# Performance work log

Measured on AMD Instinct MI355X. Metric: run time of the kernel, lower is better.

## Reference

```python
import jax, jax.numpy as jnp
import numpy as np

NUM_HEADS = 16

def _split_heads(x, H):
    B, S, D = x.shape
    return x.reshape(B, S, H, D // H).transpose(0, 2, 1, 3)  # [B,H,S,hd]

def _merge_heads(x):
    B, H, S, hd = x.shape
    return x.transpose(0, 2, 1, 3).reshape(B, S, H * hd)

def setup_inputs() -> dict:
    key = jax.random.key(0)
    k1, k2, k3, k4 = jax.random.split(key, 4)
    B, S, D = 2, 2048, 1024
    return {
        "visual_features": jax.random.normal(k1, (B, S, D), dtype=jnp.float32),
        "transaction_features": jax.random.normal(k2, (B, S, D), dtype=jnp.float32),
        "W_qkv": jax.random.normal(k3, (D, 3 * D), dtype=jnp.float32) * (1.0 / np.sqrt(D)),
        "W_out": jax.random.normal(k4, (D, D), dtype=jnp.float32) * (1.0 / np.sqrt(D)),
    }

def reference(visual_features, transaction_features, W_qkv, W_out):
    H = NUM_HEADS
    D = visual_features.shape[-1]
    scale = (D // H) ** -0.5

    v_q, v_k, v_v = [_split_heads(t, H) for t in jnp.split(visual_features @ W_qkv, 3, axis=-1)]
    t_q, t_k, t_v = [_split_heads(t, H) for t in jnp.split(transaction_features @ W_qkv, 3, axis=-1)]

    # visual queries attend to transaction keys/values (dropout = identity at eval)
    v2t = jax.nn.softmax(jnp.einsum('bhqd,bhkd->bhqk', v_q, t_k) * scale, axis=-1)
    t2v = jax.nn.softmax(jnp.einsum('bhqd,bhkd->bhqk', t_q, v_k) * scale, axis=-1)

    v2t_out = _merge_heads(jnp.einsum('bhqk,bhkd->bhqd', v2t, t_v))
    t2v_out = _merge_heads(jnp.einsum('bhqk,bhkd->bhqd', t2v, v_v))

    return (v2t_out + t2v_out) @ W_out
```

## Files before the change

### kernel.cpp

```cpp
#include <hip/hip_runtime.h>


typedef short  frag8 __attribute__((ext_vector_type(8)));
typedef float  f32x4 __attribute__((ext_vector_type(4)));

union F8 { frag8 f; uint2 u2[2]; unsigned u[4]; };

#define MFMA16(a,b,c) __builtin_amdgcn_mfma_f32_16x16x32_bf16((a),(b),(c),0,0,0)

__device__ __forceinline__ unsigned short f2bf(float f) {
  unsigned u = __builtin_bit_cast(unsigned, f);
  return (unsigned short)((u + 0x7fffu + ((u >> 16) & 1u)) >> 16);
}
__device__ __forceinline__ float bf2f(unsigned short s) {
  unsigned u = ((unsigned)s) << 16;
  return __builtin_bit_cast(float, u);
}
__device__ __forceinline__ unsigned pkbf(float lo, float hi) {
  unsigned r;
  asm("v_cvt_pk_bf16_f32 %0, %1, %2" : "=v"(r) : "v"(lo), "v"(hi));
  return r;
}
__device__ __forceinline__ float fexp2(float x) {
  float r;
  asm("v_exp_f32 %0, %1" : "=v"(r) : "v"(x));
  return r;
}

__global__ __launch_bounds__(256) void k_prep(
    const float* __restrict__ vis, const float* __restrict__ trn,
    unsigned short* __restrict__ Abf)
{
  size_t i8 = ((size_t)blockIdx.x * 256 + threadIdx.x) * 8;
  const float* src = (i8 < 4194304) ? vis + i8 : trn + (i8 - 4194304);
  float4 u = *(const float4*)src;
  float4 v = *(const float4*)(src + 4);
  uint4 w;
  w.x = pkbf(u.x, u.y); w.y = pkbf(u.z, u.w);
  w.z = pkbf(v.x, v.y); w.w = pkbf(v.z, v.w);
  *(uint4*)(Abf + i8) = w;
}

__global__ __launch_bounds__(256) void k_wt(
    const float* __restrict__ W, unsigned short* __restrict__ Wt, int N)
{
  __shared__ unsigned short L[64 * 72];
  const int tid = threadIdx.x;
  const int n0 = blockIdx.x * 64, k0 = blockIdx.y * 64;
  {
    int kr = tid >> 2, c4 = (tid & 3) * 16;
    const float* gp = W + (size_t)(k0 + kr) * N + n0 + c4;
    float4 u0 = *(const float4*)gp,       u1 = *(const float4*)(gp + 4);
    float4 u2 = *(const float4*)(gp + 8), u3 = *(const float4*)(gp + 12);
    unsigned* lw = (unsigned*)&L[kr * 72 + c4];
    lw[0] = pkbf(u0.x, u0.y); lw[1] = pkbf(u0.z, u0.w);
    lw[2] = pkbf(u1.x, u1.y); lw[3] = pkbf(u1.z, u1.w);
    lw[4] = pkbf(u2.x, u2.y); lw[5] = pkbf(u2.z, u2.w);
    lw[6] = pkbf(u3.x, u3.y); lw[7] = pkbf(u3.z, u3.w);
  }
  __syncthreads();
  int nr = tid >> 2, kc = (tid & 3) * 16;
  unsigned wb[8];
#pragma unroll
  for (int j = 0; j < 8; ++j) {
    unsigned lo = L[(kc + 2 * j)     * 72 + nr];
    unsigned hi = L[(kc + 2 * j + 1) * 72 + nr];
    wb[j] = lo | (hi << 16);
  }
  unsigned short* op = Wt + (size_t)(n0 + nr) * 1024 + k0 + kc;
  *(uint4*)op       = *(uint4*)&wb[0];
  *(uint4*)(op + 8) = *(uint4*)&wb[4];
}

__global__ __launch_bounds__(256) void k_gemm_qkv_b(
    const unsigned short* __restrict__ Abf, const unsigned short* __restrict__ WqbT,
    unsigned short* __restrict__ qkv)
{
  __shared__ unsigned short As_[128 * 32];
  __shared__ unsigned short Bs_[128 * 32];
  const int tid  = threadIdx.x;
  const int lane = tid & 63, wv = tid >> 6;
  const int lm = lane & 15, lg = lane >> 4;
  const int wg = (blockIdx.x & 7) * 192 + (blockIdx.x >> 3);
  const int nt = wg % 24, mt = wg / 24;
  const int wr = (wv >> 1) * 64, wc = (wv & 1) * 64;

  f32x4 acc[4][4] = {};

  const unsigned short* agp =
      Abf + (size_t)(mt * 128 + wv * 32 + (lane >> 2)) * 1024 + (lane & 3) * 8;
  const unsigned short* bgp =
      WqbT + (size_t)(nt * 128 + wv * 32 + (lane >> 2)) * 1024 + (lane & 3) * 8;

  for (int kt = 0; kt < 32; ++kt) {
    __syncthreads();
    __builtin_amdgcn_global_load_lds(
        (const __attribute__((address_space(1))) void*)(agp + kt * 32),
        (__attribute__((address_space(3))) void*)&As_[wv * 1024], 16, 0, 0);
    __builtin_amdgcn_global_load_lds(
        (const __attribute__((address_space(1))) void*)(agp + 16 * 1024 + kt * 32),
        (__attribute__((address_space(3))) void*)&As_[wv * 1024 + 512], 16, 0, 0);
    __builtin_amdgcn_global_load_lds(
        (const __attribute__((address_space(1))) void*)(bgp + kt * 32),
        (__attribute__((address_space(3))) void*)&Bs_[wv * 1024], 16, 0, 0);
    __builtin_amdgcn_global_load_lds(
        (const __attribute__((address_space(1))) void*)(bgp + 16 * 1024 + kt * 32),
        (__attribute__((address_space(3))) void*)&Bs_[wv * 1024 + 512], 16, 0, 0);
    __syncthreads();
    frag8 af[4], bfr[4];
#pragma unroll
    for (int mi = 0; mi < 4; ++mi)
      af[mi] = *(const frag8*)&As_[(wr + mi * 16 + lm) * 32 + lg * 8];
#pragma unroll
    for (int ni = 0; ni < 4; ++ni)
      bfr[ni] = *(const frag8*)&Bs_[(wc + ni * 16 + lm) * 32 + lg * 8];
#pragma unroll
    for (int mi = 0; mi < 4; ++mi)
#pragma unroll
      for (int ni = 0; ni < 4; ++ni)
        acc[mi][ni] = MFMA16(af[mi], bfr[ni], acc[mi][ni]);
  }

#pragma unroll
  for (int mi = 0; mi < 4; ++mi)
#pragma unroll
    for (int ni = 0; ni < 4; ++ni)
#pragma unroll
      for (int r = 0; r < 4; ++r) {
        int row = mt * 128 + wr + mi * 16 + lg * 4 + r;
        int col = nt * 128 + wc + ni * 16 + lm;
        qkv[(size_t)row * 3072 + col] = f2bf(acc[mi][ni][r]);
      }
}

__global__ __launch_bounds__(256) void k_vt(
    const unsigned short* __restrict__ qkv, unsigned short* __restrict__ Vt)
{
  __shared__ unsigned short L[64 * 72];
  const int tid = threadIdx.x;
  const int sblk = blockIdx.x;
  const int by = blockIdx.y;
  const int src = by >> 4, h = by & 15;
  {
    int sl = tid >> 2, dc = tid & 3;
    const unsigned short* gp =
        qkv + (size_t)(src * 2048 + sblk * 64 + sl) * 3072 + 2048 + h * 64 + dc * 16;
    *(frag8*)&L[sl * 72 + dc * 16]     = *(const frag8*)gp;
    *(frag8*)&L[sl * 72 + dc * 16 + 8] = *(const frag8*)(gp + 8);
  }
  __syncthreads();
  int d = tid >> 2, sc = tid & 3;
  unsigned wbuf[8];
#pragma unroll
  for (int j = 0; j < 8; ++j) {
    unsigned lo = L[(sc * 16 + 2 * j)     * 72 + d];
    unsigned hi = L[(sc * 16 + 2 * j + 1) * 72 + d];
    wbuf[j] = lo | (hi << 16);
  }
  unsigned short* op =
      Vt + ((size_t)(src * 16 + h) * 64 + d) * 2048 + sblk * 64 + sc * 16;
  *(uint4*)op       = *(uint4*)&wbuf[0];
  *(uint4*)(op + 8) = *(uint4*)&wbuf[4];
}

__global__ __launch_bounds__(256) void k_attn(
    const unsigned short* __restrict__ qkv, const unsigned short* __restrict__ Vt,
    unsigned short* __restrict__ Opart, float* __restrict__ lpart)
{
  __shared__ unsigned short Ks[2][32 * 72];
  __shared__ unsigned short Vs[2][8 * 272];
  const int tid  = threadIdx.x;
  const int lane = tid & 63, wv = tid >> 6;
  const int lm = lane & 15, lg = lane >> 4;
  const int qt = blockIdx.x, comb = blockIdx.y;
  const int dir = comb >> 5, bb = (comb >> 4) & 1, h = comb & 15;
  const int half = blockIdx.z;
  const int NT = 32, kt0 = half * 32;
  const int qbase  = (dir ? 4096 : 0) + bb * 2048;
  const int kvbase = (dir ? 0 : 4096) + bb * 2048;
  const int qcol = h * 64, kcol = 1024 + h * 64;

  const float QS = 0.125f * 1.44269504f;
  frag8 qf[2][2];
#pragma unroll
  for (int mi = 0; mi < 2; ++mi)
#pragma unroll
    for (int kb = 0; kb < 2; ++kb) {
      frag8 t = *(const frag8*)&qkv[
          (size_t)(qbase + qt * 128 + wv * 32 + mi * 16 + lm) * 3072 +
          qcol + kb * 32 + lg * 8];
#pragma unroll
      for (int j = 0; j < 8; ++j)
        t[j] = (short)f2bf(bf2f((unsigned short)t[j]) * QS);
      qf[mi][kb] = t;
    }

  f32x4 acc[2][4] = {};
  float lr[2] = {0.0f, 0.0f};

  const int skv = tid >> 3, sd = (tid & 7) * 8;
  const int vd = tid >> 2, vc = tid & 3;
  const unsigned short* __restrict__ kp =
      qkv + (size_t)(kvbase + skv) * 3072 + kcol + sd;
  const unsigned short* __restrict__ vtp =
      Vt + ((size_t)((kvbase >> 11) * 16 + h) * 64 + vd) * 2048 + vc * 8;

  frag8 Rk, Rv;

#define LOAD_R(kt_) do {                                                   \
    Rk = *(const frag8*)(kp + (size_t)(kt_) * (32 * 3072));                \
    Rv = *(const frag8*)(vtp + (size_t)(kt_) * 32);                        \
  } while (0)

#define WRITE_R(s_) do {                                                   \
    *(frag8*)&Ks[s_][skv * 72 + sd] = Rk;                                  \
    F8 tv_; tv_.f = Rv;                                                    \
    *(uint2*)&Vs[s_][(2 * vc) * 272 + vd * 4]     = tv_.u2[0];             \
    *(uint2*)&Vs[s_][(2 * vc + 1) * 272 + vd * 4] = tv_.u2[1];             \
  } while (0)

  LOAD_R(kt0);
  WRITE_R(0);
  LOAD_R(kt0 + 1);

  for (int i = 0; i < NT; ++i) {
    __syncthreads();
    if (i < NT - 1) WRITE_R((i + 1) & 1);
    if (i < NT - 2) LOAD_R(kt0 + i + 2);
    const int s = i & 1;

    frag8 kf[2][2];
#pragma unroll
    for (int t = 0; t < 2; ++t)
#pragma unroll
      for (int kb = 0; kb < 2; ++kb)
        kf[t][kb] = *(const frag8*)&Ks[s][(t * 16 + lm) * 72 + kb * 32 + lg * 8];
    f32x4 st[2][2] = {};
    __builtin_amdgcn_s_setprio(1);
#pragma unroll
    for (int mi = 0; mi < 2; ++mi)
#pragma unroll
      for (int t = 0; t < 2; ++t)
#pragma unroll
        for (int kb = 0; kb < 2; ++kb)
          st[mi][t] = MFMA16(kf[t][kb], qf[mi][kb], st[mi][t]);
    __builtin_amdgcn_s_setprio(0);

    frag8 pa[2];
#pragma unroll
    for (int mi = 0; mi < 2; ++mi) {
      f32x4 a = st[mi][0], b = st[mi][1];
      float p[8];
#pragma unroll
      for (int r = 0; r < 4; ++r) p[r]     = fexp2(a[r]);
#pragma unroll
      for (int r = 0; r < 4; ++r) p[4 + r] = fexp2(b[r]);
      lr[mi] += ((p[0] + p[1]) + (p[2] + p[3])) +
                ((p[4] + p[5]) + (p[6] + p[7]));
      F8 pk_;
      pk_.u[0] = pkbf(p[0], p[1]); pk_.u[1] = pkbf(p[2], p[3]);
      pk_.u[2] = pkbf(p[4], p[5]); pk_.u[3] = pkbf(p[6], p[7]);
      pa[mi] = pk_.f;
    }

    frag8 vb[4];
#pragma unroll
    for (int di = 0; di < 4; ++di) {
      F8 t;
      t.u2[0] = *(const uint2*)&Vs[s][lg * 272 + (di * 16 + lm) * 4];
      t.u2[1] = *(const uint2*)&Vs[s][(4 + lg) * 272 + (di * 16 + lm) * 4];
      vb[di] = t.f;
    }
    __builtin_amdgcn_s_setprio(1);
#pragma unroll
    for (int mi = 0; mi < 2; ++mi)
#pragma unroll
      for (int di = 0; di < 4; ++di)
        acc[mi][di] = MFMA16(pa[mi], vb[di], acc[mi][di]);
    __builtin_amdgcn_s_setprio(0);
  }

#undef LOAD_R
#undef WRITE_R

#pragma unroll
  for (int mi = 0; mi < 2; ++mi) {
    float l = lr[mi];
    l += __shfl_xor(l, 16);
    l += __shfl_xor(l, 32);
    int rowb = bb * 2048 + qt * 128 + wv * 32 + mi * 16;
    if (lane < 16)
      lpart[(size_t)(half * 2 + dir) * 65536 + h * 4096 + rowb + lane] = l;
#pragma unroll
    for (int r = 0; r < 4; ++r) {
      int row = rowb + lg * 4 + r;
#pragma unroll
      for (int di = 0; di < 4; ++di) {
        int col = h * 64 + di * 16 + lm;
        Opart[((size_t)(half * 2 + dir) * 4096 + row) * 1024 + col] =
            f2bf(acc[mi][di][r]);
      }
    }
  }
}

__global__ __launch_bounds__(256) void k_combine(
    const unsigned short* __restrict__ Op, const float* __restrict__ lp,
    unsigned short* __restrict__ a0, unsigned short* __restrict__ a1)
{
  int g   = blockIdx.x * 256 + threadIdx.x;
  int col = (g & 255) << 2;
  int row = (g >> 8) & 4095;
  int dir = g >> 20;
  int h   = col >> 6;
  float l = lp[(size_t)dir * 65536 + h * 4096 + row] +
            lp[(size_t)(2 + dir) * 65536 + h * 4096 + row];
  float inv = 1.0f / l;
  const unsigned short* pu = &Op[((size_t)dir * 4096 + row) * 1024 + col];
  const unsigned short* pv = &Op[((size_t)(2 + dir) * 4096 + row) * 1024 + col];
  uint2 w;
  w.x = pkbf((bf2f(pu[0]) + bf2f(pv[0])) * inv, (bf2f(pu[1]) + bf2f(pv[1])) * inv);
  w.y = pkbf((bf2f(pu[2]) + bf2f(pv[2])) * inv, (bf2f(pu[3]) + bf2f(pv[3])) * inv);
  unsigned short* dst = dir ? a1 : a0;
  *(uint2*)&dst[(size_t)row * 1024 + col] = w;
}

__global__ __launch_bounds__(256) void k_gemm_out_b(
    const unsigned short* __restrict__ x0, const unsigned short* __restrict__ x1,
    const unsigned short* __restrict__ WobT, float* __restrict__ out)
{
  __shared__ unsigned short As[128 * 40];
  __shared__ unsigned short Bs_[128 * 32];
  const int tid  = threadIdx.x;
  const int lane = tid & 63, wv = tid >> 6;
  const int lm = lane & 15, lg = lane >> 4;
  const int wg = (blockIdx.x & 7) * 32 + (blockIdx.x >> 3);
  const int nt = wg % 8, mt = wg / 8;
  const int wr = (wv >> 1) * 64, wc = (wv & 1) * 64;

  f32x4 acc[4][4] = {};

  const int am = tid >> 1, akq = (tid & 1) * 16;
  const int arow = mt * 128 + am;
  const unsigned short* __restrict__ a0p = x0 + (size_t)arow * 1024;
  const unsigned short* __restrict__ a1p = x1 + (size_t)arow * 1024;
  const unsigned short* bgp =
      WobT + (size_t)(nt * 128 + wv * 32 + (lane >> 2)) * 1024 + (lane & 3) * 8;

  for (int kt = 0; kt < 32; ++kt) {
    __syncthreads();
    __builtin_amdgcn_global_load_lds(
        (const __attribute__((address_space(1))) void*)(bgp + kt * 32),
        (__attribute__((address_space(3))) void*)&Bs_[wv * 1024], 16, 0, 0);
    __builtin_amdgcn_global_load_lds(
        (const __attribute__((address_space(1))) void*)(bgp + 16 * 1024 + kt * 32),
        (__attribute__((address_space(3))) void*)&Bs_[wv * 1024 + 512], 16, 0, 0);
    {
      frag8 u0 = *(const frag8*)(a0p + kt * 32 + akq);
      frag8 u1 = *(const frag8*)(a0p + kt * 32 + akq + 8);
      frag8 w0 = *(const frag8*)(a1p + kt * 32 + akq);
      frag8 w1 = *(const frag8*)(a1p + kt * 32 + akq + 8);
      frag8 p0, p1;
#pragma unroll
      for (int j = 0; j < 8; ++j) {
        p0[j] = (short)f2bf(bf2f((unsigned short)u0[j]) + bf2f((unsigned short)w0[j]));
        p1[j] = (short)f2bf(bf2f((unsigned short)u1[j]) + bf2f((unsigned short)w1[j]));
      }
      *(frag8*)&As[am * 40 + akq]     = p0;
      *(frag8*)&As[am * 40 + akq + 8] = p1;
    }
    __syncthreads();
    frag8 af[4], bfr[4];
#pragma unroll
    for (int mi = 0; mi < 4; ++mi)
      af[mi] = *(const frag8*)&As[(wr + mi * 16 + lm) * 40 + lg * 8];
#pragma unroll
    for (int ni = 0; ni < 4; ++ni)
      bfr[ni] = *(const frag8*)&Bs_[(wc + ni * 16 + lm) * 32 + lg * 8];
#pragma unroll
    for (int mi = 0; mi < 4; ++mi)
#pragma unroll
      for (int ni = 0; ni < 4; ++ni)
        acc[mi][ni] = MFMA16(af[mi], bfr[ni], acc[mi][ni]);
  }

#pragma unroll
  for (int mi = 0; mi < 4; ++mi)
#pragma unroll
    for (int ni = 0; ni < 4; ++ni)
#pragma unroll
      for (int r = 0; r < 4; ++r) {
        int row = mt * 128 + wr + mi * 16 + lg * 4 + r;
        int col = nt * 128 + wc + ni * 16 + lm;
        out[(size_t)row * 1024 + col] = acc[mi][ni][r];
      }
}

extern "C" void kernel_launch(void* const* d_in, const int* in_sizes, int n_in,
                              void* d_out, int out_size, void* d_ws, size_t ws_size,
                              hipStream_t stream)
{
  const float* vis  = (const float*)d_in[0];
  const float* trn  = (const float*)d_in[1];
  const float* Wqkv = (const float*)d_in[2];
  const float* Wout = (const float*)d_in[3];
  float* out = (float*)d_out;

  char* base = (char*)d_ws;
  unsigned short* qkv  = (unsigned short*)base;
  unsigned short* a0   = (unsigned short*)(base + 50331648UL);
  unsigned short* a1   = a0 + 4194304;
  unsigned short* Vt   = (unsigned short*)(base + 67108864UL);
  unsigned short* WobT = (unsigned short*)(base + 83886080UL);
  float*          lp   = (float*)(base + 85983232UL);
  unsigned short* Abf  = (unsigned short*)(base + 87031808UL);
  unsigned short* WqbT = Abf + 8388608;
  unsigned short* Op   = (unsigned short*)(base + 87031808UL);

  k_prep      <<<4096, 256, 0, stream>>>(vis, trn, Abf);
  k_wt        <<<dim3(48, 16), 256, 0, stream>>>(Wqkv, WqbT, 3072);
  k_wt        <<<dim3(16, 16), 256, 0, stream>>>(Wout, WobT, 1024);
  k_gemm_qkv_b<<<1536, 256, 0, stream>>>(Abf, WqbT, qkv);
  k_vt        <<<dim3(32, 64), 256, 0, stream>>>(qkv, Vt);
  k_attn      <<<dim3(16, 64, 2), 256, 0, stream>>>(qkv, Vt, Op, lp);
  k_combine   <<<8192, 256, 0, stream>>>(Op, lp, a0, a1);
  k_gemm_out_b<<<256, 256, 0, stream>>>(a0, a1, WobT, out);
}
```

Baseline: 240.9 us.

## Fuse prep kernels and fold split-K combine into output GEMM

Merges the input conversion and both weight transposes into one launch, and removes the separate combine kernel by having the output GEMM read the four partial attention outputs and row sums directly and normalize on load. The attention loop now advances pointers instead of recomputing offsets, and the setprio hints around the MFMAs are dropped. Fewer launches and no intermediate a0/a1 round trip, at the cost of more global loads and reciprocal math per K-step in the GEMM A-tile path.

```diff
diff --git a/kernel.cpp b/kernel.cpp
--- a/kernel.cpp
+++ b/kernel.cpp
@@ -27,26 +27,32 @@
   return r;
 }
 
-__global__ __launch_bounds__(256) void k_prep(
+__global__ __launch_bounds__(256) void k_pre(
     const float* __restrict__ vis, const float* __restrict__ trn,
-    unsigned short* __restrict__ Abf)
-{
-  size_t i8 = ((size_t)blockIdx.x * 256 + threadIdx.x) * 8;
-  const float* src = (i8 < 4194304) ? vis + i8 : trn + (i8 - 4194304);
-  float4 u = *(const float4*)src;
-  float4 v = *(const float4*)(src + 4);
-  uint4 w;
-  w.x = pkbf(u.x, u.y); w.y = pkbf(u.z, u.w);
-  w.z = pkbf(v.x, v.y); w.w = pkbf(v.z, v.w);
-  *(uint4*)(Abf + i8) = w;
-}
-
-__global__ __launch_bounds__(256) void k_wt(
-    const float* __restrict__ W, unsigned short* __restrict__ Wt, int N)
+    const float* __restrict__ Wqkv, const float* __restrict__ Wout,
+    unsigned short* __restrict__ Abf, unsigned short* __restrict__ WqbT,
+    unsigned short* __restrict__ WobT)
 {
   __shared__ unsigned short L[64 * 72];
+  const int bid = blockIdx.x;
   const int tid = threadIdx.x;
-  const int n0 = blockIdx.x * 64, k0 = blockIdx.y * 64;
+
+  if (bid < 4096) {
+    size_t i8 = ((size_t)bid * 256 + tid) * 8;
+    const float* src = (i8 < 4194304) ? vis + i8 : trn + (i8 - 4194304);
+    float4 u = *(const float4*)src;
+    float4 v = *(const float4*)(src + 4);
+    uint4 w;
+    w.x = pkbf(u.x, u.y); w.y = pkbf(u.z, u.w);
+    w.z = pkbf(v.x, v.y); w.w = pkbf(v.z, v.w);
+    *(uint4*)(Abf + i8) = w;
+    return;
+  }
+
+  const float* W; unsigned short* Wt; int N, bx, by;
+  if (bid < 4864) { int b = bid - 4096; W = Wqkv; Wt = WqbT; N = 3072; bx = b % 48; by = b / 48; }
+  else            { int b = bid - 4864; W = Wout; Wt = WobT; N = 1024; bx = b % 16; by = b / 16; }
+  const int n0 = bx * 64, k0 = by * 64;
   {
     int kr = tid >> 2, c4 = (tid & 3) * 16;
     const float* gp = W + (size_t)(k0 + kr) * N + n0 + c4;
@@ -200,16 +206,16 @@
 
   const int skv = tid >> 3, sd = (tid & 7) * 8;
   const int vd = tid >> 2, vc = tid & 3;
-  const unsigned short* __restrict__ kp =
-      qkv + (size_t)(kvbase + skv) * 3072 + kcol + sd;
-  const unsigned short* __restrict__ vtp =
-      Vt + ((size_t)((kvbase >> 11) * 16 + h) * 64 + vd) * 2048 + vc * 8;
+  const unsigned short* __restrict__ kpp =
+      qkv + (size_t)(kvbase + kt0 * 32 + skv) * 3072 + kcol + sd;
+  const unsigned short* __restrict__ vpp =
+      Vt + ((size_t)((kvbase >> 11) * 16 + h) * 64 + vd) * 2048 + kt0 * 32 + vc * 8;
 
   frag8 Rk, Rv;
 
-#define LOAD_R(kt_) do {                                                   \
-    Rk = *(const frag8*)(kp + (size_t)(kt_) * (32 * 3072));                \
-    Rv = *(const frag8*)(vtp + (size_t)(kt_) * 32);                        \
+#define LOAD_R() do {                                                      \
+    Rk = *(const frag8*)kpp;  kpp += 32 * 3072;                            \
+    Rv = *(const frag8*)vpp;  vpp += 32;                                   \
   } while (0)
 
 #define WRITE_R(s_) do {                                                   \
@@ -219,14 +225,14 @@
     *(uint2*)&Vs[s_][(2 * vc + 1) * 272 + vd * 4] = tv_.u2[1];             \
   } while (0)
 
-  LOAD_R(kt0);
+  LOAD_R();
   WRITE_R(0);
-  LOAD_R(kt0 + 1);
+  LOAD_R();
 
   for (int i = 0; i < NT; ++i) {
     __syncthreads();
     if (i < NT - 1) WRITE_R((i + 1) & 1);
-    if (i < NT - 2) LOAD_R(kt0 + i + 2);
+    if (i < NT - 2) LOAD_R();
     const int s = i & 1;
 
     frag8 kf[2][2];
@@ -236,7 +242,6 @@
       for (int kb = 0; kb < 2; ++kb)
         kf[t][kb] = *(const frag8*)&Ks[s][(t * 16 + lm) * 72 + kb * 32 + lg * 8];
     f32x4 st[2][2] = {};
-    __builtin_amdgcn_s_setprio(1);
 #pragma unroll
     for (int mi = 0; mi < 2; ++mi)
 #pragma unroll
@@ -244,7 +249,6 @@
 #pragma unroll
         for (int kb = 0; kb < 2; ++kb)
           st[mi][t] = MFMA16(kf[t][kb], qf[mi][kb], st[mi][t]);
-    __builtin_amdgcn_s_setprio(0);
 
     frag8 pa[2];
 #pragma unroll
@@ -271,13 +275,11 @@
       t.u2[1] = *(const uint2*)&Vs[s][(4 + lg) * 272 + (di * 16 + lm) * 4];
       vb[di] = t.f;
     }
-    __builtin_amdgcn_s_setprio(1);
 #pragma unroll
     for (int mi = 0; mi < 2; ++mi)
 #pragma unroll
       for (int di = 0; di < 4; ++di)
         acc[mi][di] = MFMA16(pa[mi], vb[di], acc[mi][di]);
-    __builtin_amdgcn_s_setprio(0);
   }
 
 #undef LOAD_R
@@ -304,29 +306,8 @@
   }
 }
 
-__global__ __launch_bounds__(256) void k_combine(
+__global__ __launch_bounds__(256) void k_gemm_out_b(
     const unsigned short* __restrict__ Op, const float* __restrict__ lp,
-    unsigned short* __restrict__ a0, unsigned short* __restrict__ a1)
-{
-  int g   = blockIdx.x * 256 + threadIdx.x;
-  int col = (g & 255) << 2;
-  int row = (g >> 8) & 4095;
-  int dir = g >> 20;
-  int h   = col >> 6;
-  float l = lp[(size_t)dir * 65536 + h * 4096 + row] +
-            lp[(size_t)(2 + dir) * 65536 + h * 4096 + row];
-  float inv = 1.0f / l;
-  const unsigned short* pu = &Op[((size_t)dir * 4096 + row) * 1024 + col];
-  const unsigned short* pv = &Op[((size_t)(2 + dir) * 4096 + row) * 1024 + col];
-  uint2 w;
-  w.x = pkbf((bf2f(pu[0]) + bf2f(pv[0])) * inv, (bf2f(pu[1]) + bf2f(pv[1])) * inv);
-  w.y = pkbf((bf2f(pu[2]) + bf2f(pv[2])) * inv, (bf2f(pu[3]) + bf2f(pv[3])) * inv);
-  unsigned short* dst = dir ? a1 : a0;
-  *(uint2*)&dst[(size_t)row * 1024 + col] = w;
-}
-
-__global__ __launch_bounds__(256) void k_gemm_out_b(
-    const unsigned short* __restrict__ x0, const unsigned short* __restrict__ x1,
     const unsigned short* __restrict__ WobT, float* __restrict__ out)
 {
   __shared__ unsigned short As[128 * 40];
@@ -342,8 +323,10 @@
 
   const int am = tid >> 1, akq = (tid & 1) * 16;
   const int arow = mt * 128 + am;
-  const unsigned short* __restrict__ a0p = x0 + (size_t)arow * 1024;
-  const unsigned short* __restrict__ a1p = x1 + (size_t)arow * 1024;
+  const unsigned short* __restrict__ p00 = Op + (size_t)arow * 1024;
+  const unsigned short* __restrict__ p01 = p00 + (size_t)4096 * 1024;
+  const unsigned short* __restrict__ p10 = p00 + (size_t)2 * 4096 * 1024;
+  const unsigned short* __restrict__ p11 = p00 + (size_t)3 * 4096 * 1024;
   const unsigned short* bgp =
       WobT + (size_t)(nt * 128 + wv * 32 + (lane >> 2)) * 1024 + (lane & 3) * 8;
 
@@ -356,18 +339,30 @@
         (const __attribute__((address_space(1))) void*)(bgp + 16 * 1024 + kt * 32),
         (__attribute__((address_space(3))) void*)&Bs_[wv * 1024 + 512], 16, 0, 0);
     {
-      frag8 u0 = *(const frag8*)(a0p + kt * 32 + akq);
-      frag8 u1 = *(const frag8*)(a0p + kt * 32 + akq + 8);
-      frag8 w0 = *(const frag8*)(a1p + kt * 32 + akq);
-      frag8 w1 = *(const frag8*)(a1p + kt * 32 + akq + 8);
-      frag8 p0, p1;
+      const int kcol = kt * 32 + akq;
+      const int hh = kt >> 1;
+      float inv0 = 1.0f / (lp[hh * 4096 + arow]          + lp[131072 + hh * 4096 + arow]);
+      float inv1 = 1.0f / (lp[65536 + hh * 4096 + arow]  + lp[196608 + hh * 4096 + arow]);
+      frag8 u0 = *(const frag8*)(p00 + kcol);
+      frag8 u1 = *(const frag8*)(p00 + kcol + 8);
+      frag8 v0 = *(const frag8*)(p10 + kcol);
+      frag8 v1 = *(const frag8*)(p10 + kcol + 8);
+      frag8 w0 = *(const frag8*)(p01 + kcol);
+      frag8 w1 = *(const frag8*)(p01 + kcol + 8);
+      frag8 x0 = *(const frag8*)(p11 + kcol);
+      frag8 x1 = *(const frag8*)(p11 + kcol + 8);
+      frag8 q0, q1;
 #pragma unroll
       for (int j = 0; j < 8; ++j) {
-        p0[j] = (short)f2bf(bf2f((unsigned short)u0[j]) + bf2f((unsigned short)w0[j]));
-        p1[j] = (short)f2bf(bf2f((unsigned short)u1[j]) + bf2f((unsigned short)w1[j]));
+        float a0 = (bf2f((unsigned short)u0[j]) + bf2f((unsigned short)v0[j])) * inv0 +
+                   (bf2f((unsigned short)w0[j]) + bf2f((unsigned short)x0[j])) * inv1;
+        float a1 = (bf2f((unsigned short)u1[j]) + bf2f((unsigned short)v1[j])) * inv0 +
+                   (bf2f((unsigned short)w1[j]) + bf2f((unsigned short)x1[j])) * inv1;
+        q0[j] = (short)f2bf(a0);
+        q1[j] = (short)f2bf(a1);
       }
-      *(frag8*)&As[am * 40 + akq]     = p0;
-      *(frag8*)&As[am * 40 + akq + 8] = p1;
+      *(frag8*)&As[am * 40 + akq]     = q0;
+      *(frag8*)&As[am * 40 + akq + 8] = q1;
     }
     __syncthreads();
     frag8 af[4], bfr[4];
@@ -408,8 +403,6 @@
 
   char* base = (char*)d_ws;
   unsigned short* qkv  = (unsigned short*)base;
-  unsigned short* a0   = (unsigned short*)(base + 50331648UL);
-  unsigned short* a1   = a0 + 4194304;
   unsigned short* Vt   = (unsigned short*)(base + 67108864UL);
   unsigned short* WobT = (unsigned short*)(base + 83886080UL);
   float*          lp   = (float*)(base + 85983232UL);
@@ -417,12 +410,9 @@
   unsigned short* WqbT = Abf + 8388608;
   unsigned short* Op   = (unsigned short*)(base + 87031808UL);
 
-  k_prep      <<<4096, 256, 0, stream>>>(vis, trn, Abf);
-  k_wt        <<<dim3(48, 16), 256, 0, stream>>>(Wqkv, WqbT, 3072);
-  k_wt        <<<dim3(16, 16), 256, 0, stream>>>(Wout, WobT, 1024);
+  k_pre       <<<5120, 256, 0, stream>>>(vis, trn, Wqkv, Wout, Abf, WqbT, WobT);
   k_gemm_qkv_b<<<1536, 256, 0, stream>>>(Abf, WqbT, qkv);
   k_vt        <<<dim3(32, 64), 256, 0, stream>>>(qkv, Vt);
   k_attn      <<<dim3(16, 64, 2), 256, 0, stream>>>(qkv, Vt, Op, lp);
-  k_combine   <<<8192, 256, 0, stream>>>(Op, lp, a0, a1);
-  k_gemm_out_b<<<256, 256, 0, stream>>>(a0, a1, WobT, out);
-}
+  k_gemm_out_b<<<256, 256, 0, stream>>>(Op, lp, WobT, out);
+}
```

After: 236.2 us. No clear change (-1.9%).
